# Performance work log

Hardware: AMD Instinct MI355X
Metric: run time of the kernel (lower is better)

Reference implementation:

```python
import jax, jax.numpy as jnp
import numpy as np

NUM_HEADS = 16

def setup_inputs() -> dict:
    key = jax.random.key(0)
    ks = jax.random.split(key, 6)
    B, S, D = 2, 2048, 1024
    return {
        "hidden_states": jax.random.normal(ks[0], (B, S, D), dtype=jnp.float32),
        "c_attn_w": jax.random.normal(ks[1], (D, 3 * D), dtype=jnp.float32) * 0.02,
        "c_attn_b": jax.random.normal(ks[2], (3 * D,), dtype=jnp.float32) * 0.02,
        "attn_bias": jax.random.normal(ks[3], (S, S), dtype=jnp.float32) * 0.02,
        "c_proj_w": jax.random.normal(ks[4], (D, D), dtype=jnp.float32) * 0.02,
        "c_proj_b": jax.random.normal(ks[5], (D,), dtype=jnp.float32) * 0.02,
    }

def reference(hidden_states, c_attn_w, c_attn_b, attn_bias, c_proj_w, c_proj_b):
    B, S, D = hidden_states.shape
    H = NUM_HEADS
    hd = D // H
    # fused QKV projection: [B,S,3D]
    qkv = hidden_states @ c_attn_w + c_attn_b
    q, k, v = jnp.split(qkv, 3, axis=-1)
    # [B,H,S,hd]
    q = q.reshape(B, S, H, hd).transpose(0, 2, 1, 3)
    k = k.reshape(B, S, H, hd).transpose(0, 2, 1, 3)
    v = v.reshape(B, S, H, hd).transpose(0, 2, 1, 3)
    # scores [B,H,S,S] with learned additive bias and causal mask
    scores = jnp.einsum('bhqd,bhkd->bhqk', q, k) / jnp.sqrt(jnp.float32(hd))
    scores = scores + attn_bias[:S, :S][None, None, :, :]
    causal = jnp.tril(jnp.ones((S, S), dtype=bool))
    scores = jnp.where(causal[None, None, :, :], scores, jnp.float32(-1e9))
    attn = jax.nn.softmax(scores, axis=-1)
    ctx = jnp.einsum('bhqk,bhkd->bhqd', attn, v)
    ctx = ctx.transpose(0, 2, 1, 3).reshape(B, S, D)
    out = ctx @ c_proj_w + c_proj_b  # resid dropout is identity in eval
    return (out, k, v)
```

## Files before the change

### kernel.cpp

```cpp
#include <hip/hip_runtime.h>
#include <hip/hip_bf16.h>
#include <stdint.h>


typedef __attribute__((ext_vector_type(4))) float f32x4;
typedef __attribute__((ext_vector_type(16))) float f32x16;
typedef __attribute__((ext_vector_type(8))) short s16x8;
typedef __attribute__((ext_vector_type(4))) short s16x4;
typedef unsigned short u16;

#define LOG2E 1.4426950408889634f
#define QSCALE 0.18033688011112042f

__device__ __forceinline__ u16 f2bf(float f) {
  unsigned w;
  asm("v_cvt_pk_bf16_f32 %0, %1, %2" : "=v"(w) : "v"(f), "v"(f));
  return (u16)w;
}
__device__ __forceinline__ unsigned cvtpk(float lo, float hi) {
  unsigned w;
  asm("v_cvt_pk_bf16_f32 %0, %1, %2" : "=v"(w) : "v"(lo), "v"(hi));
  return w;
}
__device__ __forceinline__ float bf2f(u16 h) {
  unsigned int x = ((unsigned int)h) << 16;
  return __builtin_bit_cast(float, x);
}
__device__ __forceinline__ float fexp2(float x) {
  float r;
  asm("v_exp_f32 %0, %1" : "=v"(r) : "v"(x));
  return r;
}
__device__ __forceinline__ void pl32swap(unsigned& a, unsigned& b) {
  asm volatile("v_permlane32_swap_b32 %0, %1" : "+v"(a), "+v"(b));
}
__device__ __forceinline__ s16x8 frag8(unsigned a, unsigned b, unsigned c, unsigned d) {
  union { unsigned u[4]; s16x8 v; } t;
  t.u[0] = a; t.u[1] = b; t.u[2] = c; t.u[3] = d;
  return t.v;
}
__device__ __forceinline__ f32x16 mfma32(s16x8 a, s16x8 b, f32x16 c) {
  return __builtin_amdgcn_mfma_f32_32x32x16_bf16(a, b, c, 0, 0, 0);
}

__device__ __forceinline__ void gload_lds16(const u16* g, u16* lds) {
  __builtin_amdgcn_global_load_lds(
      (const __attribute__((address_space(1))) unsigned int*)g,
      (__attribute__((address_space(3))) unsigned int*)lds, 16, 0, 0);
}


__global__ __launch_bounds__(256) void cvt_f32_bf16(const float* __restrict__ x,
                                                    u16* __restrict__ y, int n4) {
  int i = blockIdx.x * 256 + threadIdx.x;
  if (i < n4) {
    f32x4 v = *(const f32x4*)&x[(size_t)i * 4];
    s16x4 o;
    o[0] = (short)f2bf(v[0]); o[1] = (short)f2bf(v[1]);
    o[2] = (short)f2bf(v[2]); o[3] = (short)f2bf(v[3]);
    *(s16x4*)&y[(size_t)i * 4] = o;
  }
}

__global__ __launch_bounds__(256) void transpose_w_bf16(const float* __restrict__ W,
                                                        u16* __restrict__ WT,
                                                        int K, int N) {
  __shared__ float tile[32][33];
  const int n0 = blockIdx.x * 32, k0 = blockIdx.y * 32;
  const int tx = threadIdx.x & 31, ty = threadIdx.x >> 5;
#pragma unroll
  for (int i = 0; i < 32; i += 8)
    tile[ty + i][tx] = W[(size_t)(k0 + ty + i) * N + (n0 + tx)];
  __syncthreads();
#pragma unroll
  for (int i = 0; i < 32; i += 8)
    WT[(size_t)(n0 + ty + i) * K + (k0 + tx)] = f2bf(tile[tx][ty + i]);
}

__global__ __launch_bounds__(256) void transpose_v(const u16* __restrict__ v,
                                                   u16* __restrict__ vT) {
  __shared__ u16 tile[64][72];
  const int bh = blockIdx.y;
  const int s0 = blockIdx.x * 64;
  const int tr = threadIdx.x >> 2, tc = (threadIdx.x & 3) * 16;
  const u16* src = v + (size_t)bh * 131072u + (size_t)(s0 + tr) * 64 + tc;
  *(s16x8*)&tile[tr][tc] = *(const s16x8*)src;
  *(s16x8*)&tile[tr][tc + 8] = *(const s16x8*)(src + 8);
  __syncthreads();
  u16 o[16];
#pragma unroll
  for (int x = 0; x < 16; x++) o[x] = tile[tc + x][tr];
  u16* dst = vT + (size_t)bh * 131072u + (size_t)tr * 2048 + s0 + tc;
  *(s16x8*)dst = *(s16x8*)&o[0];
  *(s16x8*)(dst + 8) = *(s16x8*)&o[8];
}

__global__ __launch_bounds__(128) void bias_tile(const float* __restrict__ B,
                                                 u16* __restrict__ T) {
  const int kt = blockIdx.x;
  const int q32 = blockIdx.y;
  if (kt > (q32 >> 1)) return;
  const int t = threadIdx.x >> 6, lane = threadIdx.x & 63;
  const int hh = q32 >> 1;
  const size_t boff = (size_t)(hh + (q32 & 1)) * (hh + 1);
  const int q = q32 * 32 + (lane & 31);
  const int kb = kt * 64 + t * 32 + 4 * (lane >> 5);
  u16 v[16];
#pragma unroll
  for (int r = 0; r < 16; r++) {
    const int k = kb + (r & 3) + 8 * (r >> 2);
    v[r] = (k <= q) ? f2bf(B[(size_t)q * 2048 + k] * LOG2E) : (u16)0xFF80;
  }
  u16* dst = T + (boff + kt) * 2048 + t * 1024 + (size_t)lane * 16;
  *(s16x8*)dst = *(s16x8*)&v[0];
  *(s16x8*)(dst + 8) = *(s16x8*)&v[8];
}


template <int MODE>
__global__ __launch_bounds__(256) void gemm_bt(
    const u16* __restrict__ A, const u16* __restrict__ BT,
    const float* __restrict__ bias, float* __restrict__ outF,
    u16* __restrict__ q_ws, u16* __restrict__ k_ws, u16* __restrict__ v_ws,
    int M, int N, int K) {
  __shared__ u16 As[2][128 * 32];
  __shared__ u16 Bs[2][128 * 32];
  const int nwg = gridDim.x * gridDim.y;
  int flat = blockIdx.y * gridDim.x + blockIdx.x;
  flat = (flat & 7) * (nwg >> 3) + (flat >> 3);
  const int m0 = (flat / gridDim.x) * 128, n0 = (flat % gridDim.x) * 128;
  const int tid = threadIdx.x;
  const int wid = tid >> 6, lane = tid & 63;
  const int c = lane & 15, hi = lane >> 4;
  const int wm = wid >> 1, wn = wid & 1;
  const int srow = lane >> 2;
  const int skp = (lane & 3) * 8;

  f32x4 acc[4][4] = {};

#define STG(SLOT, K0)                                                         \
  {                                                                           \
    _Pragma("unroll")                                                         \
    for (int t = 0; t < 2; t++) {                                             \
      const int rowl = wid * 32 + t * 16;                                     \
      gload_lds16(&A[(size_t)(m0 + rowl + srow) * K + (K0) + skp],            \
                  &As[SLOT][rowl * 32]);                                      \
      gload_lds16(&BT[(size_t)(n0 + rowl + srow) * K + (K0) + skp],           \
                  &Bs[SLOT][rowl * 32]);                                      \
    }                                                                         \
  }

  STG(0, 0);
  __syncthreads();

  int bufi = 0;
  for (int k0 = 0; k0 < K; k0 += 32) {
    if (k0 + 32 < K) {
      if (bufi) { STG(0, k0 + 32); } else { STG(1, k0 + 32); }
    }
    s16x8 af[4], bfr[4];
#pragma unroll
    for (int i = 0; i < 4; i++)
      af[i] = *(const s16x8*)&As[bufi][(wm * 64 + i * 16 + c) * 32 + hi * 8];
#pragma unroll
    for (int i = 0; i < 4; i++)
      bfr[i] = *(const s16x8*)&Bs[bufi][(wn * 64 + i * 16 + c) * 32 + hi * 8];
    __builtin_amdgcn_s_setprio(1);
#pragma unroll
    for (int i = 0; i < 4; i++)
#pragma unroll
      for (int j = 0; j < 4; j++)
        acc[i][j] = __builtin_amdgcn_mfma_f32_16x16x32_bf16(af[i], bfr[j], acc[i][j], 0, 0, 0);
    __builtin_amdgcn_s_setprio(0);
    __syncthreads();
    bufi ^= 1;
  }
#undef STG

  if (MODE == 1) {
#pragma unroll
    for (int i = 0; i < 4; i++) {
#pragma unroll
      for (int j = 0; j < 4; j++) {
        const int col = n0 + wn * 64 + j * 16 + c;
        const int rb = m0 + wm * 64 + i * 16 + hi * 4;
        const float bv = bias[col];
#pragma unroll
        for (int u = 0; u < 4; u++)
          outF[(size_t)(rb + u) * N + col] = acc[i][j][u] + bv;
      }
    }
  } else {
    const int which = n0 >> 10;
#pragma unroll
    for (int i = 0; i < 4; i++) {
#pragma unroll
      for (int j = 0; j < 4; j++) {
        const int col = n0 + wn * 64 + j * 16 + c;
        const int rb = m0 + wm * 64 + i * 16 + hi * 4;
        const float bv = bias[col];
        const int h = (col >> 6) & 15, d = col & 63;
#pragma unroll
        for (int u = 0; u < 4; u++) {
          const int r = rb + u;
          const int b = r >> 11, s = r & 2047;
          const size_t idx = (size_t)(b * 16 + h) * 131072u + (size_t)s * 64 + d;
          const float v = acc[i][j][u] + bv;
          if (which == 0) {
            q_ws[idx] = f2bf(v * QSCALE);
          } else if (which == 1) {
            outF[4194304u + idx] = v;
            k_ws[idx] = f2bf(v);
          } else {
            outF[8388608u + idx] = v;
            v_ws[idx] = f2bf(v);
          }
        }
      }
    }
  }
}


__global__ __launch_bounds__(256, 4) void attn_fused(
    const u16* __restrict__ q_ws, const u16* __restrict__ k_ws,
    const u16* __restrict__ vT_ws, const u16* __restrict__ biasT,
    u16* __restrict__ ctx) {
  __shared__ u16 Ks[2][64 * 64];
  __shared__ u16 Vs[2][64 * 64];

  const int id = blockIdx.x;
  const int bh = (id & 7) * 4 + ((id >> 3) & 3);
  const int j = id >> 5, j0 = j & 7, sg = j >> 3;
  const int qblk = (sg == 0) ? j0 : (sg == 1) ? (15 - j0)
                 : (sg == 2) ? (16 + j0) : (31 - j0);

  const int wid = threadIdx.x >> 6, lane = threadIdx.x & 63;
  const int pq = wid >> 1, par = wid & 1;
  const int l31 = lane & 31, hi5 = lane >> 5;
  const int qrow0 = qblk * 64 + pq * 32;

  const u16* qh = q_ws + (size_t)bh * 131072u;
  const u16* kh = k_ws + (size_t)bh * 131072u;
  const u16* vh = vT_ws + (size_t)bh * 131072u;

  s16x8 qf[4];
#pragma unroll
  for (int s = 0; s < 4; s++)
    qf[s] = *(const s16x8*)&qh[(size_t)(qrow0 + l31) * 64 + s * 16 + hi5 * 8];

  const int q32 = qblk * 2 + pq;
  const int hh = q32 >> 1;
  const size_t boff = (size_t)(hh + (q32 & 1)) * (hh + 1);
  const u16* bbase = biasT + boff * 2048 + (size_t)par * 1024 + (size_t)lane * 16;

  const int sl_r = lane >> 3, sl_c = lane & 7;

  f32x16 o0 = {}, o1 = {};
  float mrow = -1e30f, lpart = 0.f;

#define STAGE(BUF, N0)                                                        \
  {                                                                           \
    _Pragma("unroll")                                                         \
    for (int t = 0; t < 2; t++) {                                             \
      const int rb = wid * 16 + t * 8;                                        \
      const int r = rb + sl_r;                                                \
      gload_lds16(&kh[(size_t)((N0) + r) * 64 + ((sl_c ^ (r & 7)) * 8)],      \
                  &Ks[BUF][rb * 64]);                                         \
      gload_lds16(&vh[(size_t)r * 2048 + (N0) + ((sl_c ^ (r & 7)) * 8)],      \
                  &Vs[BUF][rb * 64]);                                         \
    }                                                                         \
  }

  STAGE(0, 0);
  __syncthreads();

  int buf = 0;
  const int nkt = qblk + 1;
  const int swz = l31 & 7;
  const int arow = par * 32 + l31;

  s16x8 bc0 = *(const s16x8*)(bbase);
  s16x8 bc1 = *(const s16x8*)(bbase + 8);

  for (int kt = 0; kt < nkt; ++kt) {
    if (kt + 1 < nkt) {
      if (buf) { STAGE(0, kt * 64 + 64); } else { STAGE(1, kt * 64 + 64); }
    }
    const u16* btn = bbase + (size_t)((kt + 1 < nkt) ? kt + 1 : kt) * 2048;
    const s16x8 bn0 = *(const s16x8*)(btn);
    const s16x8 bn1 = *(const s16x8*)(btn + 8);

    f32x16 s0;
#pragma unroll
    for (int r = 0; r < 8; r++) {
      s0[r] = bf2f((u16)bc0[r]);
      s0[r + 8] = bf2f((u16)bc1[r]);
    }

    const u16* ksb = &Ks[buf][0];
    __builtin_amdgcn_s_setprio(1);
#pragma unroll
    for (int s = 0; s < 4; s++) {
      const int chq = ((s * 2 + hi5) ^ swz) * 8;
      const s16x8 a0 = *(const s16x8*)&ksb[arow * 64 + chq];
      s0 = mfma32(a0, qf[s], s0);
    }
    __builtin_amdgcn_s_setprio(0);

    float t0 = fmaxf(fmaxf(s0[0], s0[1]), fmaxf(s0[2], s0[3]));
    float t1 = fmaxf(fmaxf(s0[4], s0[5]), fmaxf(s0[6], s0[7]));
    float t2 = fmaxf(fmaxf(s0[8], s0[9]), fmaxf(s0[10], s0[11]));
    float t3 = fmaxf(fmaxf(s0[12], s0[13]), fmaxf(s0[14], s0[15]));
    float tm = fmaxf(fmaxf(t0, t1), fmaxf(t2, t3));
    tm = fmaxf(tm, __shfl_xor(tm, 32));

    if (__any(tm > mrow + 8.f)) {
      const float nm = fmaxf(mrow, tm);
      const float al = fexp2(mrow - nm);
      mrow = nm;
      lpart *= al;
#pragma unroll
      for (int r = 0; r < 16; r++) { o0[r] *= al; o1[r] *= al; }
    }

    float a0s = 0.f, a1s = 0.f;
#pragma unroll
    for (int r = 0; r < 8; r++) {
      s0[r] = fexp2(s0[r] - mrow);       a0s += s0[r];
      s0[r + 8] = fexp2(s0[r + 8] - mrow); a1s += s0[r + 8];
    }
    lpart += a0s + a1s;

    unsigned wv0 = cvtpk(s0[0], s0[1]),   wv1 = cvtpk(s0[2], s0[3]);
    unsigned wv2 = cvtpk(s0[4], s0[5]),   wv3 = cvtpk(s0[6], s0[7]);
    unsigned wv4 = cvtpk(s0[8], s0[9]),   wv5 = cvtpk(s0[10], s0[11]);
    unsigned wv6 = cvtpk(s0[12], s0[13]), wv7 = cvtpk(s0[14], s0[15]);
    pl32swap(wv0, wv2); pl32swap(wv1, wv3);
    pl32swap(wv4, wv6); pl32swap(wv5, wv7);

    const u16* vsb = &Vs[buf][0];
    __builtin_amdgcn_s_setprio(1);
#pragma unroll
    for (int hf = 0; hf < 2; hf++) {
      const s16x8 pa = hf ? frag8(wv4, wv5, wv6, wv7) : frag8(wv0, wv1, wv2, wv3);
      const int s = par * 2 + hf;
      const int chv = ((s * 2 + hi5) ^ swz) * 8;
      const s16x8 v0 = *(const s16x8*)&vsb[l31 * 64 + chv];
      const s16x8 v1 = *(const s16x8*)&vsb[(32 + l31) * 64 + chv];
      o0 = mfma32(pa, v0, o0);
      o1 = mfma32(pa, v1, o1);
    }
    __builtin_amdgcn_s_setprio(0);

    __syncthreads();
    buf ^= 1;
    bc0 = bn0; bc1 = bn1;
  }
#undef STAGE

  lpart += __shfl_xor(lpart, 32);

  float* obuf = (float*)&Ks[0][0];
  float2* mlb = (float2*)&Vs[0][0];

  __syncthreads();
  if (hi5 == 0) mlb[(par * 2 + pq) * 64 + l31] = make_float2(mrow, lpart);
  if (par == 1) {
    const int slot = pq * 64 + lane;
#pragma unroll
    for (int r = 0; r < 16; r++) {
      obuf[r * 128 + slot] = o0[r];
      obuf[(16 + r) * 128 + slot] = o1[r];
    }
  }
  __syncthreads();
  if (par == 0) {
    const int slot = pq * 64 + lane;
    const int b = bh >> 4, h = bh & 15;
#pragma unroll
    for (int r = 0; r < 16; r++) {
      const int qloc = (r & 3) + 8 * (r >> 2) + 4 * hi5;
      const float2 Aml = mlb[pq * 64 + qloc];
      const float2 Bml = mlb[(2 + pq) * 64 + qloc];
      const float mm = fmaxf(Aml.x, Bml.x);
      const float fa = fexp2(Aml.x - mm), fb = fexp2(Bml.x - mm);
      const float inv = __builtin_amdgcn_rcpf(Aml.y * fa + Bml.y * fb);
      const float om0 = (o0[r] * fa + obuf[r * 128 + slot] * fb) * inv;
      const float om1 = (o1[r] * fa + obuf[(16 + r) * 128 + slot] * fb) * inv;
      const int tok = b * 2048 + qrow0 + qloc;
      ctx[(size_t)tok * 1024 + h * 64 + l31] = f2bf(om0);
      ctx[(size_t)tok * 1024 + h * 64 + 32 + l31] = f2bf(om1);
    }
  }
}


extern "C" void kernel_launch(void* const* d_in, const int* in_sizes, int n_in,
                              void* d_out, int out_size, void* d_ws, size_t ws_size,
                              hipStream_t stream) {
  const float* hs        = (const float*)d_in[0];
  const float* c_attn_w  = (const float*)d_in[1];
  const float* c_attn_b  = (const float*)d_in[2];
  const float* attn_bias = (const float*)d_in[3];
  const float* c_proj_w  = (const float*)d_in[4];
  const float* c_proj_b  = (const float*)d_in[5];
  float* out = (float*)d_out;

  uint8_t* ws = (uint8_t*)d_ws;
  u16* hsb    = (u16*)(ws + 0);
  u16* wqkvT  = (u16*)(ws + 8388608u);
  u16* wprojT = (u16*)(ws + 14680064u);
  u16* q_ws   = (u16*)(ws + 16777216u);
  u16* k_ws   = (u16*)(ws + 25165824u);
  u16* vT_ws  = (u16*)(ws + 33554432u);
  u16* ctx    = (u16*)(ws + 41943040u);
  u16* v_ws   = ctx;
  u16* biasT  = hsb;

  cvt_f32_bf16<<<4096, 256, 0, stream>>>(hs, hsb, 1048576);
  transpose_w_bf16<<<dim3(96, 32), 256, 0, stream>>>(c_attn_w, wqkvT, 1024, 3072);
  transpose_w_bf16<<<dim3(32, 32), 256, 0, stream>>>(c_proj_w, wprojT, 1024, 1024);

  gemm_bt<0><<<dim3(24, 32), 256, 0, stream>>>(hsb, wqkvT, c_attn_b, out,
                                               q_ws, k_ws, v_ws, 4096, 3072, 1024);

  transpose_v<<<dim3(32, 32), 256, 0, stream>>>(v_ws, vT_ws);

  bias_tile<<<dim3(32, 64), 128, 0, stream>>>(attn_bias, biasT);

  attn_fused<<<dim3(1024), 256, 0, stream>>>(q_ws, k_ws, vT_ws, biasT, ctx);

  gemm_bt<1><<<dim3(8, 32), 256, 0, stream>>>(ctx, wprojT, c_proj_b, out,
                                              (u16*)nullptr, (u16*)nullptr, (u16*)nullptr,
                                              4096, 1024, 1024);
}
```

Before: 132.9 us.

## Replace QKV GEMM with 256x256-tile, 8-wave kernel using swizzled LDS and staged loads

Adds a dedicated QKV projection kernel that uses 256x256 output tiles, 512 threads, K-step 64, an XOR-swizzled LDS layout and direct global-to-LDS loads. The next K-tile's loads are interleaved with the four MFMA phases under explicit barriers and waitcnts. The goal is higher data reuse per tile and better overlap of memory with MFMA than the 128x128 kernel gave. The trade-off is heavy LDS use (128KB), only 192 workgroups, and a hand-tuned schedule. The output projection GEMM is de-templated into a single plain-output kernel.

```diff
diff --git a/kernel.cpp b/kernel.cpp
--- a/kernel.cpp
+++ b/kernel.cpp
@@ -117,11 +117,142 @@
 }
 
 
-template <int MODE>
+__global__ __launch_bounds__(512, 2) void gemm_qkv8(
+    const u16* __restrict__ A, const u16* __restrict__ BT,
+    const float* __restrict__ bias, float* __restrict__ outF,
+    u16* __restrict__ q_ws, u16* __restrict__ k_ws, u16* __restrict__ v_ws) {
+  __shared__ u16 As[2][256 * 64];
+  __shared__ u16 Bs[2][256 * 64];
+
+  const int flat0 = blockIdx.x;
+  const int flat = (flat0 & 7) * 24 + (flat0 >> 3);
+  const int m0 = (flat / 12) * 256;
+  const int n0 = (flat % 12) * 256;
+
+  const int tid = threadIdx.x;
+  const int wid = tid >> 6, lane = tid & 63;
+  const int c16 = lane & 15, hi4 = lane >> 4;
+  const int wm = wid >> 2, wn = wid & 3;
+
+  const int srow = wid * 8 + (lane >> 3);
+  const int sch = ((lane & 7) ^ (lane >> 3)) * 8;
+
+#define STGA(S, KT, H)                                                          \
+  gload_lds16(&A[(size_t)(m0 + (H) * 128 + srow) * 1024 + (KT) * 64 + sch],     \
+              &As[S][(H) * 8192 + wid * 512]);                                  \
+  gload_lds16(&A[(size_t)(m0 + (H) * 128 + 64 + srow) * 1024 + (KT) * 64 + sch],\
+              &As[S][(H) * 8192 + 4096 + wid * 512]);
+#define STGB(S, KT, H)                                                          \
+  gload_lds16(&BT[(size_t)(n0 + (H) * 128 + srow) * 1024 + (KT) * 64 + sch],    \
+              &Bs[S][(H) * 8192 + wid * 512]);                                  \
+  gload_lds16(&BT[(size_t)(n0 + (H) * 128 + 64 + srow) * 1024 + (KT) * 64 + sch],\
+              &Bs[S][(H) * 8192 + 4096 + wid * 512]);
+
+  f32x4 acc[8][4] = {};
+
+  STGA(0, 0, 0); STGA(0, 0, 1); STGB(0, 0, 0); STGB(0, 0, 1);
+
+  const int ch0 = (hi4 ^ (c16 & 7)) * 8;
+  const int ch1 = ((4 + hi4) ^ (c16 & 7)) * 8;
+  const int arow = wm * 128 + c16;
+  const int brow = wn * 64 + c16;
+
+  s16x8 af[4], bfr[4];
+
+#define DSRD_B(CH)                                                              \
+  _Pragma("unroll")                                                             \
+  for (int j = 0; j < 4; j++)                                                   \
+    bfr[j] = *(const s16x8*)&bs[(brow + j * 16) * 64 + (CH)];
+#define DSRD_A(ILO, CH)                                                         \
+  _Pragma("unroll")                                                             \
+  for (int i = 0; i < 4; i++)                                                   \
+    af[i] = *(const s16x8*)&as[(arow + ((ILO) + i) * 16) * 64 + (CH)];
+#define MFMA16(IB)                                                              \
+  __builtin_amdgcn_s_setprio(1);                                                \
+  _Pragma("unroll")                                                             \
+  for (int i = 0; i < 4; i++)                                                   \
+    _Pragma("unroll")                                                           \
+    for (int j = 0; j < 4; j++)                                                 \
+      acc[(IB) + i][j] =                                                        \
+          __builtin_amdgcn_mfma_f32_16x16x32_bf16(af[i], bfr[j], acc[(IB)+i][j],\
+                                                  0, 0, 0);                     \
+  __builtin_amdgcn_s_setprio(0);
+#define LGKM0                                                                   \
+  asm volatile("s_waitcnt lgkmcnt(0)" ::: "memory");                            \
+  __builtin_amdgcn_sched_barrier(0);
+
+  for (int t = 0; t < 16; ++t) {
+    const int cur = t & 1, nxt = cur ^ 1;
+    const u16* as = &As[cur][0];
+    const u16* bs = &Bs[cur][0];
+
+    if (t < 15) { STGA(nxt, t + 1, 0); }
+    if (t < 15) { asm volatile("s_waitcnt vmcnt(2)" ::: "memory"); }
+    else        { asm volatile("s_waitcnt vmcnt(0)" ::: "memory"); }
+    __builtin_amdgcn_s_barrier();
+    DSRD_B(ch0); DSRD_A(0, ch0);
+    __builtin_amdgcn_s_barrier();
+    LGKM0; MFMA16(0);
+    __builtin_amdgcn_s_barrier();
+
+    if (t < 15) { STGA(nxt, t + 1, 1); }
+    DSRD_A(4, ch0);
+    __builtin_amdgcn_s_barrier();
+    LGKM0; MFMA16(4);
+    __builtin_amdgcn_s_barrier();
+
+    if (t < 15) { STGB(nxt, t + 1, 0); }
+    DSRD_B(ch1); DSRD_A(0, ch1);
+    __builtin_amdgcn_s_barrier();
+    LGKM0; MFMA16(0);
+    __builtin_amdgcn_s_barrier();
+
+    if (t < 15) { STGB(nxt, t + 1, 1); }
+    DSRD_A(4, ch1);
+    __builtin_amdgcn_s_barrier();
+    LGKM0; MFMA16(4);
+    __builtin_amdgcn_s_barrier();
+  }
+#undef STGA
+#undef STGB
+#undef DSRD_A
+#undef DSRD_B
+#undef MFMA16
+#undef LGKM0
+
+  const int which = n0 >> 10;
+#pragma unroll
+  for (int i = 0; i < 8; i++) {
+#pragma unroll
+    for (int j = 0; j < 4; j++) {
+      const int col = n0 + wn * 64 + j * 16 + c16;
+      const int rb = m0 + wm * 128 + i * 16 + hi4 * 4;
+      const float bv = bias[col];
+      const int h = (col >> 6) & 15, d = col & 63;
+#pragma unroll
+      for (int u = 0; u < 4; u++) {
+        const int r = rb + u;
+        const int b = r >> 11, s = r & 2047;
+        const size_t idx = (size_t)(b * 16 + h) * 131072u + (size_t)s * 64 + d;
+        const float v = acc[i][j][u] + bv;
+        if (which == 0) {
+          q_ws[idx] = f2bf(v * QSCALE);
+        } else if (which == 1) {
+          outF[4194304u + idx] = v;
+          k_ws[idx] = f2bf(v);
+        } else {
+          outF[8388608u + idx] = v;
+          v_ws[idx] = f2bf(v);
+        }
+      }
+    }
+  }
+}
+
+
 __global__ __launch_bounds__(256) void gemm_bt(
     const u16* __restrict__ A, const u16* __restrict__ BT,
     const float* __restrict__ bias, float* __restrict__ outF,
-    u16* __restrict__ q_ws, u16* __restrict__ k_ws, u16* __restrict__ v_ws,
     int M, int N, int K) {
   __shared__ u16 As[2][128 * 32];
   __shared__ u16 Bs[2][128 * 32];
@@ -177,46 +308,16 @@
   }
 #undef STG
 
-  if (MODE == 1) {
-#pragma unroll
-    for (int i = 0; i < 4; i++) {
-#pragma unroll
-      for (int j = 0; j < 4; j++) {
-        const int col = n0 + wn * 64 + j * 16 + c;
-        const int rb = m0 + wm * 64 + i * 16 + hi * 4;
-        const float bv = bias[col];
-#pragma unroll
-        for (int u = 0; u < 4; u++)
-          outF[(size_t)(rb + u) * N + col] = acc[i][j][u] + bv;
-      }
-    }
-  } else {
-    const int which = n0 >> 10;
-#pragma unroll
-    for (int i = 0; i < 4; i++) {
-#pragma unroll
-      for (int j = 0; j < 4; j++) {
-        const int col = n0 + wn * 64 + j * 16 + c;
-        const int rb = m0 + wm * 64 + i * 16 + hi * 4;
-        const float bv = bias[col];
-        const int h = (col >> 6) & 15, d = col & 63;
-#pragma unroll
-        for (int u = 0; u < 4; u++) {
-          const int r = rb + u;
-          const int b = r >> 11, s = r & 2047;
-          const size_t idx = (size_t)(b * 16 + h) * 131072u + (size_t)s * 64 + d;
-          const float v = acc[i][j][u] + bv;
-          if (which == 0) {
-            q_ws[idx] = f2bf(v * QSCALE);
-          } else if (which == 1) {
-            outF[4194304u + idx] = v;
-            k_ws[idx] = f2bf(v);
-          } else {
-            outF[8388608u + idx] = v;
-            v_ws[idx] = f2bf(v);
-          }
-        }
-      }
+#pragma unroll
+  for (int i = 0; i < 4; i++) {
+#pragma unroll
+    for (int j = 0; j < 4; j++) {
+      const int col = n0 + wn * 64 + j * 16 + c;
+      const int rb = m0 + wm * 64 + i * 16 + hi * 4;
+      const float bv = bias[col];
+#pragma unroll
+      for (int u = 0; u < 4; u++)
+        outF[(size_t)(rb + u) * N + col] = acc[i][j][u] + bv;
     }
   }
 }
@@ -422,8 +523,8 @@
   transpose_w_bf16<<<dim3(96, 32), 256, 0, stream>>>(c_attn_w, wqkvT, 1024, 3072);
   transpose_w_bf16<<<dim3(32, 32), 256, 0, stream>>>(c_proj_w, wprojT, 1024, 1024);
 
-  gemm_bt<0><<<dim3(24, 32), 256, 0, stream>>>(hsb, wqkvT, c_attn_b, out,
-                                               q_ws, k_ws, v_ws, 4096, 3072, 1024);
+  gemm_qkv8<<<dim3(192), 512, 0, stream>>>(hsb, wqkvT, c_attn_b, out,
+                                           q_ws, k_ws, v_ws);
 
   transpose_v<<<dim3(32, 32), 256, 0, stream>>>(v_ws, vT_ws);
 
@@ -431,7 +532,6 @@
 
   attn_fused<<<dim3(1024), 256, 0, stream>>>(q_ws, k_ws, vT_ws, biasT, ctx);
 
-  gemm_bt<1><<<dim3(8, 32), 256, 0, stream>>>(ctx, wprojT, c_proj_b, out,
-                                              (u16*)nullptr, (u16*)nullptr, (u16*)nullptr,
-                                              4096, 1024, 1024);
-}
+  gemm_bt<<<dim3(8, 32), 256, 0, stream>>>(ctx, wprojT, c_proj_b, out,
+                                           4096, 1024, 1024);
+}
```

Result: slower. 148.2 us (+11.5%).
